# Kernel tuning notes

Hardware: AMD Instinct MI355X
Metric: run time of the kernel (lower is better)

## Reference

```python
import jax, jax.numpy as jnp
import numpy as np

B, C, N = 4, 256, 512
CQ = C // 4
SIGMA = 15.0
PICK = 0  # args.picked_point_num
FACTOR = 180.0 / (np.pi * SIGMA)
BN_EPS = 1e-5


def _angle_embed(angles, W, b):
    """SinusoidalPositionalEmbedding (interleaved sin/cos, detached) + Linear proj."""
    d = W.shape[0]
    div_term = jnp.exp(jnp.arange(0, d, 2, dtype=jnp.float32) * (-np.log(10000.0) / d))
    omegas = (angles * FACTOR)[..., None] * div_term  # (..., d/2)
    # torch cat([sin, cos], dim=2) on (-1, d/2, 1) then view -> interleaved [s0,c0,s1,c1,...]
    emb = jnp.stack([jnp.sin(omegas), jnp.cos(omegas)], axis=-1).reshape(*angles.shape, d)
    emb = jax.lax.stop_gradient(emb)  # .detach() in torch
    return emb @ W.T + b


def setup_inputs() -> dict:
    key = jax.random.key(0)
    ks = jax.random.split(key, 16)
    s = 0.05
    return {
        "x": jax.random.normal(ks[0], (B, C, N), jnp.float32),
        "pca": jax.random.normal(ks[1], (B, C, N), jnp.float32),
        "angle_lrf": jax.random.uniform(ks[2], (B, N, N), jnp.float32, 0.0, np.pi),
        "angle_pca": jax.random.uniform(ks[3], (B, N), jnp.float32, 0.0, np.pi),
        "Wkp": jax.random.normal(ks[4], (CQ, C), jnp.float32) * s,
        "Wk": jax.random.normal(ks[5], (CQ, C), jnp.float32) * s,
        "Wv": jax.random.normal(ks[6], (C, C), jnp.float32) * s,
        "Wvp": jax.random.normal(ks[7], (C, C), jnp.float32) * s,
        "emb1_W": jax.random.normal(ks[8], (CQ, CQ), jnp.float32) * s,
        "emb1_b": jnp.zeros((CQ,), jnp.float32),
        "emb2_W": jax.random.normal(ks[9], (CQ, CQ), jnp.float32) * s,
        "emb2_b": jnp.zeros((CQ,), jnp.float32),
        "lin_W": jax.random.normal(ks[10], (C, C), jnp.float32) * s,
        "lin_b": jnp.zeros((C,), jnp.float32),
        "bn_gamma": jnp.ones((C,), jnp.float32),
        "bn_beta": jnp.zeros((C,), jnp.float32),
    }


def reference(x, pca, angle_lrf, angle_pca, Wkp, Wk, Wv, Wvp,
              emb1_W, emb1_b, emb2_W, emb2_b, lin_W, lin_b, bn_gamma, bn_beta):
    # q uses the k_conv_pca weight (weight tying in __init__)
    x_q = jnp.einsum('oc,bcn->bno', Wkp, x)            # (B,N,CQ)
    k_lrf = jnp.einsum('oc,bcn->bon', Wk, x)           # (B,CQ,N)
    k_pca = jnp.einsum('oc,bcn->bon', Wkp, pca)        # (B,CQ,N)
    energy_lrf = jnp.einsum('bno,bom->bnm', x_q, k_lrf)
    energy_pca = jnp.einsum('bno,bom->bnm', x_q, k_pca)
    e1 = _angle_embed(angle_lrf, emb1_W, emb1_b)       # (B,N,N,CQ) relative-angle bias
    energy_lrf = energy_lrf + jnp.einsum('bnc,bnmc->bnm', x_q, e1)
    e2 = _angle_embed(angle_pca, emb2_W, emb2_b)       # (B,N,CQ)
    energy_pca = energy_pca + jnp.einsum('bnc,bmc->bnm', x_q, e2)
    energy = jax.nn.softmax(energy_lrf + energy_pca, axis=-1)
    # extra column renormalization
    energy = energy / (1e-12 + energy.sum(axis=1, keepdims=True))
    point_relation = energy[:, PICK:PICK + 1, :]       # (B,1,N)
    v_lrf = jnp.einsum('oc,bcn->bon', Wv, x)
    v_pca = jnp.einsum('oc,bcn->bon', Wvp, pca)
    x_lrf = jnp.einsum('bon,bnm->bom', v_lrf, energy)
    x_pca = jnp.einsum('bon,bnm->bom', v_pca, energy)
    x_r = 0.5 * x_lrf + 0.5 * x_pca
    z = jnp.einsum('oc,bcn->bon', lin_W, x - x_r) + lin_b[None, :, None]
    # BatchNorm1d (training-mode batch stats, biased var)
    mu = z.mean(axis=(0, 2), keepdims=True)
    var = z.var(axis=(0, 2), keepdims=True)
    y = bn_gamma[None, :, None] * (z - mu) * jax.lax.rsqrt(var + BN_EPS) + bn_beta[None, :, None]
    out = x + jax.nn.gelu(y, approximate=False)
    return out, point_relation
```

## Files before the change

### kernel.cpp

```cpp
#include <hip/hip_runtime.h>
#include <math.h>

#define FCT_REV 0.6079271018540267f
#define DIVK 0.28782313662425575f

using bf16x8 = __attribute__((ext_vector_type(8))) short;
using f32x4  = __attribute__((ext_vector_type(4))) float;

__device__ inline short f2bf(float f) {
    union { float f; unsigned u; } v; v.f = f;
    unsigned r = v.u + 0x7FFFu + ((v.u >> 16) & 1u);
    return (short)(r >> 16);
}
__device__ inline float bf2f(short s) {
    union { unsigned u; float f; } v;
    v.u = ((unsigned)(unsigned short)s) << 16;
    return v.f;
}
__device__ inline unsigned pk2(float lo, float hi) {
    return ((unsigned)(unsigned short)f2bf(hi) << 16) | (unsigned)(unsigned short)f2bf(lo);
}
__device__ inline float sinrev(float x) {
    float r; asm("v_sin_f32 %0, %1" : "=v"(r) : "v"(x)); return r;
}
__device__ inline float cosrev(float x) {
    float r; asm("v_cos_f32 %0, %1" : "=v"(r) : "v"(x)); return r;
}

__global__ __launch_bounds__(256) void k_prep(
    const float* __restrict__ Wkp, const float* __restrict__ Wk,
    const float* __restrict__ Wv, const float* __restrict__ Wvp,
    const float* __restrict__ linW, const float* __restrict__ e1W,
    const float* __restrict__ e2W,
    const float* __restrict__ x, const float* __restrict__ pca,
    short* __restrict__ Wcatb, short* __restrict__ InTb,
    float* __restrict__ e2Wt, float* __restrict__ stat, float* __restrict__ colsum)
{
    __shared__ float ts[64][65];
    const int bid = blockIdx.x;
    const int t = threadIdx.x;
    if (bid < 176) {
        if (bid == 0) {
            for (int i = t; i < 2048; i += 256) colsum[i] = 0.f;
            for (int i = t; i < 512; i += 256) stat[i] = 0.f;
        } else if (bid == 1) {
            for (int i = t; i < 4096; i += 256) {
                int k = i >> 6, o = i & 63;
                e2Wt[k*64 + o] = e2W[o*64 + k];
            }
        }
        #pragma unroll
        for (int rr = 0; rr < 4; ++rr) {
            const int r = bid*4 + rr;
            for (int k = t; k < 512; k += 256) {
                float v = 0.f;
                if (r < 64) { if (k < 256) v = Wkp[r*256 + k]; }
                else if (r < 128) { int o = r-64;  v = (k<256) ? Wk[o*256+k]  : Wkp[o*256 + k-256]; }
                else if (r < 384) { int o = r-128; v = (k<256) ? Wv[o*256+k]  : Wvp[o*256 + k-256]; }
                else if (r < 640) { int o = r-384; if (k<256) v = linW[o*256+k]; }
                else {
                    int o = r-640;
                    if (k < 256) {
                        float a = 0.f;
                        for (int j = 0; j < 64; ++j) a = fmaf(e1W[j*64 + o], Wkp[j*256 + k], a);
                        v = a;
                    }
                }
                Wcatb[(size_t)r*512 + k] = f2bf(v);
            }
        }
    } else {
        const int id = bid - 176;
        const int b  = id >> 6;
        const int kt = (id >> 3) & 7;
        const int nt = id & 7;
        const int k0 = kt*64, n0 = nt*64;
        const float* src = (k0 < 256) ? (x + ((size_t)b*256 + k0)*512)
                                      : (pca + ((size_t)b*256 + (k0-256))*512);
        #pragma unroll
        for (int i = 0; i < 16; ++i) {
            int idx = t + 256*i;
            int r = idx >> 6, c = idx & 63;
            ts[r][c] = src[(size_t)r*512 + n0 + c];
        }
        __syncthreads();
        short* dst = InTb + (size_t)b*512*512;
        #pragma unroll
        for (int i = 0; i < 16; ++i) {
            int idx = t + 256*i;
            int n = idx >> 6, k = idx & 63;
            dst[(size_t)(n0+n)*512 + k0 + k] = f2bf(ts[k][n]);
        }
    }
}

__global__ __launch_bounds__(256) void k_gemm1(
    const short* __restrict__ Wcatb, const short* __restrict__ InTb,
    const float* __restrict__ angle_pca, const float* __restrict__ e2Wt,
    short* __restrict__ xqb, short* __restrict__ KtT, short* __restrict__ vsumb,
    float* __restrict__ linx, float* __restrict__ q1T)
{
    __shared__ float embs[32][65];
    __shared__ float e2ws[64][64];
    const int bid = blockIdx.x;
    const int b  = bid / 176;
    const int rt = (bid / 16) % 11;
    const int ct = bid % 16;
    const int r0 = rt*64, c0 = ct*32;
    const int w = threadIdx.x >> 6, lane = threadIdx.x & 63;
    const int lr = lane & 15, lg = lane >> 4;
    const int t = threadIdx.x;

    if (r0 == 64) {
        const int mloc = t >> 3, q = t & 7;
        const float arev = angle_pca[b*512 + c0 + mloc] * FCT_REV;
        #pragma unroll
        for (int j = q*4; j < q*4+4; ++j) {
            const float arg = arev * __expf(-(float)j * DIVK);
            embs[mloc][2*j]   = sinrev(arg);
            embs[mloc][2*j+1] = cosrev(arg);
        }
        #pragma unroll
        for (int i = 0; i < 16; ++i) {
            const int idx = t + 256*i;
            e2ws[idx >> 6][idx & 63] = e2Wt[idx];
        }
    }

    const short* ap  = Wcatb + (size_t)(r0 + w*16 + lr)*512 + 8*lg;
    const short* bp0 = InTb + (size_t)b*512*512 + (size_t)(c0 + lr)*512 + 8*lg;
    const short* bp1 = bp0 + 16*512;

    f32x4 acc0 = {0.f,0.f,0.f,0.f}, acc1 = {0.f,0.f,0.f,0.f};
    #pragma unroll 4
    for (int kk = 0; kk < 512; kk += 32) {
        bf16x8 a  = *(const bf16x8*)(ap  + kk);
        bf16x8 b0 = *(const bf16x8*)(bp0 + kk);
        bf16x8 b1 = *(const bf16x8*)(bp1 + kk);
        acc0 = __builtin_amdgcn_mfma_f32_16x16x32_bf16(a, b0, acc0, 0, 0, 0);
        acc1 = __builtin_amdgcn_mfma_f32_16x16x32_bf16(a, b1, acc1, 0, 0, 0);
    }
    const int rowb = r0 + w*16 + lg*4;
    const int col0 = c0 + lr;
    if (r0 == 0) {
        #pragma unroll
        for (int j = 0; j < 4; ++j) {
            xqb[((size_t)b*512 + col0)*64 + rowb + j]      = f2bf(acc0[j]);
            xqb[((size_t)b*512 + col0 + 16)*64 + rowb + j] = f2bf(acc1[j]);
        }
    } else if (r0 == 64) {
        __syncthreads();
        const int o0 = w*16 + lg*4;
        float e[8];
        #pragma unroll
        for (int i = 0; i < 8; ++i) e[i] = 0.f;
        #pragma unroll 8
        for (int k = 0; k < 64; ++k) {
            const float em0 = embs[lr][k];
            const float em1 = embs[lr + 16][k];
            #pragma unroll
            for (int j = 0; j < 4; ++j) {
                const float wv = e2ws[k][o0 + j];
                e[j]     = fmaf(wv, em0, e[j]);
                e[4 + j] = fmaf(wv, em1, e[4 + j]);
            }
        }
        uint2 u0, u1;
        u0.x = pk2(acc0[0] + e[0], acc0[1] + e[1]);
        u0.y = pk2(acc0[2] + e[2], acc0[3] + e[3]);
        u1.x = pk2(acc1[0] + e[4], acc1[1] + e[5]);
        u1.y = pk2(acc1[2] + e[6], acc1[3] + e[7]);
        *(uint2*)(KtT + ((size_t)b*512 + col0)*64 + o0)      = u0;
        *(uint2*)(KtT + ((size_t)b*512 + col0 + 16)*64 + o0) = u1;
    } else if (r0 < 384) {
        #pragma unroll
        for (int j = 0; j < 4; ++j) {
            vsumb[((size_t)b*256 + rowb-128 + j)*512 + col0]      = f2bf(acc0[j]);
            vsumb[((size_t)b*256 + rowb-128 + j)*512 + col0 + 16] = f2bf(acc1[j]);
        }
    } else if (r0 < 640) {
        #pragma unroll
        for (int j = 0; j < 4; ++j) {
            linx[((size_t)b*256 + rowb-384 + j)*512 + col0]      = acc0[j];
            linx[((size_t)b*256 + rowb-384 + j)*512 + col0 + 16] = acc1[j];
        }
    } else {
        #pragma unroll
        for (int j = 0; j < 4; ++j) {
            q1T[((size_t)b*512 + col0)*64 + rowb-640 + j]      = acc0[j];
            q1T[((size_t)b*512 + col0 + 16)*64 + rowb-640 + j] = acc1[j];
        }
    }
}

__global__ __launch_bounds__(256) void k_qk(
    const short* __restrict__ xqb, const short* __restrict__ KtT,
    float* __restrict__ S)
{
    const int bid = blockIdx.x;
    const int b  = bid / 128;
    const int rt = (bid / 16) % 8;
    const int ct = bid % 16;
    const int r0 = rt*64, c0 = ct*32;
    const int w = threadIdx.x >> 6, lane = threadIdx.x & 63;
    const int lr = lane & 15, lg = lane >> 4;
    const short* ap  = xqb + ((size_t)b*512 + r0 + w*16 + lr)*64 + 8*lg;
    const short* bp0 = KtT + ((size_t)b*512 + c0 + lr)*64 + 8*lg;
    const short* bp1 = bp0 + 16*64;
    f32x4 acc0 = {0.f,0.f,0.f,0.f}, acc1 = {0.f,0.f,0.f,0.f};
    #pragma unroll
    for (int kk = 0; kk < 64; kk += 32) {
        bf16x8 a  = *(const bf16x8*)(ap  + kk);
        bf16x8 b0 = *(const bf16x8*)(bp0 + kk);
        bf16x8 b1 = *(const bf16x8*)(bp1 + kk);
        acc0 = __builtin_amdgcn_mfma_f32_16x16x32_bf16(a, b0, acc0, 0, 0, 0);
        acc1 = __builtin_amdgcn_mfma_f32_16x16x32_bf16(a, b1, acc1, 0, 0, 0);
    }
    const int rowb = r0 + w*16 + lg*4;
    const int col0 = c0 + lr;
    float* Sb = S + (size_t)b*512*512;
    #pragma unroll
    for (int j = 0; j < 4; ++j) {
        Sb[(size_t)(rowb+j)*512 + col0]      = acc0[j];
        Sb[(size_t)(rowb+j)*512 + col0 + 16] = acc1[j];
    }
}

__global__ __launch_bounds__(256) void k_energy2(
    const float* __restrict__ S, const float* __restrict__ q1T,
    const float* __restrict__ angle_lrf, short* __restrict__ ETb,
    float* __restrict__ colsum)
{
    const int b  = blockIdx.x >> 7;
    const int n0 = (blockIdx.x & 127) * 4;
    __shared__ float qs[4][64];
    __shared__ float divs[32];
    __shared__ float4 xw[4];
    const int t = threadIdx.x;
    if (t < 64) {
        #pragma unroll
        for (int i = 0; i < 4; ++i) qs[i][t] = q1T[((size_t)b*512 + n0 + i)*64 + t];
    } else if (t < 96) {
        divs[t-64] = __expf(-(float)(t-64) * DIVK);
    }
    __syncthreads();
    float acc[4][2], av[4][2];
    #pragma unroll
    for (int i = 0; i < 4; ++i) {
        const float2 sv = *(const float2*)&S[((size_t)b*512 + n0 + i)*512 + 2*t];
        const float2 an = *(const float2*)&angle_lrf[((size_t)b*512 + n0 + i)*512 + 2*t];
        acc[i][0] = sv.x; acc[i][1] = sv.y;
        av[i][0] = an.x * FCT_REV; av[i][1] = an.y * FCT_REV;
    }
    #pragma unroll 2
    for (int j = 0; j < 32; ++j) {
        const float d = divs[j];
        #pragma unroll
        for (int i = 0; i < 4; ++i) {
            const float q0 = qs[i][2*j], q1 = qs[i][2*j+1];
            #pragma unroll
            for (int m = 0; m < 2; ++m) {
                const float arg = av[i][m] * d;
                acc[i][m] = fmaf(q0, sinrev(arg), fmaf(q1, cosrev(arg), acc[i][m]));
            }
        }
    }
    float v0 = fmaxf(acc[0][0], acc[0][1]), v1 = fmaxf(acc[1][0], acc[1][1]);
    float v2 = fmaxf(acc[2][0], acc[2][1]), v3 = fmaxf(acc[3][0], acc[3][1]);
    #pragma unroll
    for (int off = 1; off < 64; off <<= 1) {
        v0 = fmaxf(v0, __shfl_xor(v0, off));
        v1 = fmaxf(v1, __shfl_xor(v1, off));
        v2 = fmaxf(v2, __shfl_xor(v2, off));
        v3 = fmaxf(v3, __shfl_xor(v3, off));
    }
    const int wid = t >> 6, lane = t & 63;
    if (lane == 0) { float4 f = {v0,v1,v2,v3}; xw[wid] = f; }
    __syncthreads();
    {
        const float4 a0 = xw[0], a1 = xw[1], a2 = xw[2], a3 = xw[3];
        v0 = fmaxf(fmaxf(a0.x,a1.x), fmaxf(a2.x,a3.x));
        v1 = fmaxf(fmaxf(a0.y,a1.y), fmaxf(a2.y,a3.y));
        v2 = fmaxf(fmaxf(a0.z,a1.z), fmaxf(a2.z,a3.z));
        v3 = fmaxf(fmaxf(a0.w,a1.w), fmaxf(a2.w,a3.w));
    }
    float p[4][2];
    p[0][0] = __expf(acc[0][0]-v0); p[0][1] = __expf(acc[0][1]-v0);
    p[1][0] = __expf(acc[1][0]-v1); p[1][1] = __expf(acc[1][1]-v1);
    p[2][0] = __expf(acc[2][0]-v2); p[2][1] = __expf(acc[2][1]-v2);
    p[3][0] = __expf(acc[3][0]-v3); p[3][1] = __expf(acc[3][1]-v3);
    float s0 = p[0][0]+p[0][1], s1 = p[1][0]+p[1][1];
    float s2 = p[2][0]+p[2][1], s3 = p[3][0]+p[3][1];
    #pragma unroll
    for (int off = 1; off < 64; off <<= 1) {
        s0 += __shfl_xor(s0, off); s1 += __shfl_xor(s1, off);
        s2 += __shfl_xor(s2, off); s3 += __shfl_xor(s3, off);
    }
    __syncthreads();
    if (lane == 0) { float4 f = {s0,s1,s2,s3}; xw[wid] = f; }
    __syncthreads();
    {
        const float4 a0 = xw[0], a1 = xw[1], a2 = xw[2], a3 = xw[3];
        s0 = (a0.x+a1.x) + (a2.x+a3.x);
        s1 = (a0.y+a1.y) + (a2.y+a3.y);
        s2 = (a0.z+a1.z) + (a2.z+a3.z);
        s3 = (a0.w+a1.w) + (a2.w+a3.w);
    }
    const float i0 = 1.f/s0, i1 = 1.f/s1, i2 = 1.f/s2, i3 = 1.f/s3;
    short* Eb = ETb + (size_t)b*512*512;
    #pragma unroll
    for (int m = 0; m < 2; ++m) {
        const float e0 = p[0][m]*i0, e1 = p[1][m]*i1, e2 = p[2][m]*i2, e3 = p[3][m]*i3;
        uint2 u;
        u.x = pk2(e0, e1);
        u.y = pk2(e2, e3);
        *(uint2*)(Eb + (size_t)(2*t + m)*512 + n0) = u;
        atomicAdd(&colsum[b*512 + 2*t + m], (e0 + e1) + (e2 + e3));
    }
}

__global__ __launch_bounds__(256) void k_xr2(
    const short* __restrict__ vsumb, const short* __restrict__ ETb,
    const float* __restrict__ colsum, short* __restrict__ xrT,
    float* __restrict__ out)
{
    const int bid = blockIdx.x;
    const int b  = bid / 64;
    const int rt = (bid / 16) % 4;
    const int ct = bid % 16;
    const int r0 = rt*64, c0 = ct*32;
    const int w = threadIdx.x >> 6, lane = threadIdx.x & 63;
    const int lr = lane & 15, lg = lane >> 4;
    const short* ap  = vsumb + (size_t)b*256*512 + (size_t)(r0 + w*16 + lr)*512 + 8*lg;
    const short* bp0 = ETb + (size_t)b*512*512 + (size_t)(c0 + lr)*512 + 8*lg;
    const short* bp1 = bp0 + 16*512;
    f32x4 acc0 = {0.f,0.f,0.f,0.f}, acc1 = {0.f,0.f,0.f,0.f};
    #pragma unroll 4
    for (int kk = 0; kk < 512; kk += 32) {
        bf16x8 a  = *(const bf16x8*)(ap  + kk);
        bf16x8 b0 = *(const bf16x8*)(bp0 + kk);
        bf16x8 b1 = *(const bf16x8*)(bp1 + kk);
        acc0 = __builtin_amdgcn_mfma_f32_16x16x32_bf16(a, b0, acc0, 0, 0, 0);
        acc1 = __builtin_amdgcn_mfma_f32_16x16x32_bf16(a, b1, acc1, 0, 0, 0);
    }
    const int rowb = r0 + w*16 + lg*4;
    const int m0 = c0 + lr, m1 = m0 + 16;
    const float rc0 = 1.f / (1e-12f + colsum[b*512 + m0]);
    const float rc1 = 1.f / (1e-12f + colsum[b*512 + m1]);
    const float s0 = 0.5f * rc0, s1 = 0.5f * rc1;
    short* xb = xrT + (size_t)b*512*256;
    uint2 u;
    u.x = pk2(acc0[0]*s0, acc0[1]*s0);
    u.y = pk2(acc0[2]*s0, acc0[3]*s0);
    *(uint2*)(xb + (size_t)m0*256 + rowb) = u;
    u.x = pk2(acc1[0]*s1, acc1[1]*s1);
    u.y = pk2(acc1[2]*s1, acc1[3]*s1);
    *(uint2*)(xb + (size_t)m1*256 + rowb) = u;
    if (w == 0 && lg == 0) {
        out[(size_t)4*256*512 + b*512 + m0] = bf2f(ETb[((size_t)b*512 + m0)*512]) * rc0;
        out[(size_t)4*256*512 + b*512 + m1] = bf2f(ETb[((size_t)b*512 + m1)*512]) * rc1;
    }
}

__global__ __launch_bounds__(256) void k_z2st(
    const short* __restrict__ Wcatb, const short* __restrict__ xrT,
    const float* __restrict__ linx, const float* __restrict__ lin_b,
    float* __restrict__ z, float* __restrict__ stat)
{
    const int bid = blockIdx.x;
    const int b  = bid / 64;
    const int rt = (bid / 16) % 4;
    const int ct = bid % 16;
    const int r0 = rt*64, c0 = ct*32;
    const int w = threadIdx.x >> 6, lane = threadIdx.x & 63;
    const int lr = lane & 15, lg = lane >> 4;
    const short* ap  = Wcatb + (size_t)(384 + r0 + w*16 + lr)*512 + 8*lg;
    const short* bp0 = xrT + (size_t)b*512*256 + (size_t)(c0 + lr)*256 + 8*lg;
    const short* bp1 = bp0 + 16*256;
    f32x4 acc0 = {0.f,0.f,0.f,0.f}, acc1 = {0.f,0.f,0.f,0.f};
    #pragma unroll
    for (int kk = 0; kk < 256; kk += 32) {
        bf16x8 a  = *(const bf16x8*)(ap  + kk);
        bf16x8 b0 = *(const bf16x8*)(bp0 + kk);
        bf16x8 b1 = *(const bf16x8*)(bp1 + kk);
        acc0 = __builtin_amdgcn_mfma_f32_16x16x32_bf16(a, b0, acc0, 0, 0, 0);
        acc1 = __builtin_amdgcn_mfma_f32_16x16x32_bf16(a, b1, acc1, 0, 0, 0);
    }
    const int rowb = r0 + w*16 + lg*4;
    const int col0 = c0 + lr;
    const float* Lb = linx + (size_t)b*256*512;
    float* zb = z + (size_t)b*256*512;
    #pragma unroll
    for (int j = 0; j < 4; ++j) {
        const float lb = lin_b[rowb+j];
        const float z0 = Lb[(size_t)(rowb+j)*512 + col0]      - acc0[j] + lb;
        const float z1 = Lb[(size_t)(rowb+j)*512 + col0 + 16] - acc1[j] + lb;
        zb[(size_t)(rowb+j)*512 + col0]      = z0;
        zb[(size_t)(rowb+j)*512 + col0 + 16] = z1;
        float s  = z0 + z1;
        float s2 = z0*z0 + z1*z1;
        #pragma unroll
        for (int off = 1; off < 16; off <<= 1) {
            s  += __shfl_xor(s,  off);
            s2 += __shfl_xor(s2, off);
        }
        if (lr == 0) {
            atomicAdd(&stat[rowb+j], s);
            atomicAdd(&stat[256 + rowb+j], s2);
        }
    }
}

__global__ __launch_bounds__(256) void k_final(
    const float* __restrict__ x, const float* __restrict__ z,
    const float* __restrict__ stat, const float* __restrict__ gamma,
    const float* __restrict__ beta, float* __restrict__ out)
{
    const int gid = blockIdx.x*256 + threadIdx.x;
    const int base = gid * 4;
    const int c = (base >> 9) & 255;
    const float mu  = stat[c] * (1.f/2048.f);
    const float var = stat[256 + c] * (1.f/2048.f) - mu*mu;
    const float gsc = gamma[c] * rsqrtf(var + 1e-5f);
    const float bt  = beta[c];
    const float4 zv = *(const float4*)&z[base];
    const float4 xv = *(const float4*)&x[base];
    float4 ov;
    {
        float y = (zv.x - mu)*gsc + bt;
        ov.x = xv.x + 0.5f*y*(1.f + erff(y*0.70710678118654752f));
        y = (zv.y - mu)*gsc + bt;
        ov.y = xv.y + 0.5f*y*(1.f + erff(y*0.70710678118654752f));
        y = (zv.z - mu)*gsc + bt;
        ov.z = xv.z + 0.5f*y*(1.f + erff(y*0.70710678118654752f));
        y = (zv.w - mu)*gsc + bt;
        ov.w = xv.w + 0.5f*y*(1.f + erff(y*0.70710678118654752f));
    }
    *(float4*)&out[base] = ov;
}

extern "C" void kernel_launch(void* const* d_in, const int* in_sizes, int n_in,
                              void* d_out, int out_size, void* d_ws, size_t ws_size,
                              hipStream_t stream)
{
    const float* x         = (const float*)d_in[0];
    const float* pca       = (const float*)d_in[1];
    const float* angle_lrf = (const float*)d_in[2];
    const float* angle_pca = (const float*)d_in[3];
    const float* Wkp       = (const float*)d_in[4];
    const float* Wk        = (const float*)d_in[5];
    const float* Wv        = (const float*)d_in[6];
    const float* Wvp       = (const float*)d_in[7];
    const float* e1W       = (const float*)d_in[8];
    const float* e2W       = (const float*)d_in[10];
    const float* linW      = (const float*)d_in[12];
    const float* linb      = (const float*)d_in[13];
    const float* gamma     = (const float*)d_in[14];
    const float* beta      = (const float*)d_in[15];

    char* w = (char*)d_ws;
    short* Wcatb  = (short*)(w + 0);
    short* InTb   = (short*)(w + 720896);
    short* vsumb  = (short*)(w + 2818048);
    short* KtT    = (short*)(w + 3866624);
    short* ETb    = (short*)(w + 4128768);
    short* xrT    = (short*)(w + 6225920);
    float* stat   = (float*)(w + 7274496);
    float* colsum = (float*)(w + 7276544);
    float* S      = (float*)(w + 7284736);
    float* e2Wt   = (float*)(w + 7284736);
    float* z      = (float*)(w + 7284736);
    short* xqb    = (short*)(w + 12003328);
    float* q1T    = (float*)(w + 12265472);
    float* linx   = (float*)(w + 12789760);
    float* out    = (float*)d_out;

    k_prep   <<<432, 256, 0, stream>>>(Wkp, Wk, Wv, Wvp, linW, e1W, e2W, x, pca,
                                       Wcatb, InTb, e2Wt, stat, colsum);
    k_gemm1  <<<704, 256, 0, stream>>>(Wcatb, InTb, angle_pca, e2Wt,
                                       xqb, KtT, vsumb, linx, q1T);
    k_qk     <<<512, 256, 0, stream>>>(xqb, KtT, S);
    k_energy2<<<512, 256, 0, stream>>>(S, q1T, angle_lrf, ETb, colsum);
    k_xr2    <<<256, 256, 0, stream>>>(vsumb, ETb, colsum, xrT, out);
    k_z2st   <<<256, 256, 0, stream>>>(Wcatb, xrT, linx, linb, z, stat);
    k_final  <<<512, 256, 0, stream>>>(x, z, stat, gamma, beta, out);
}
```

Baseline: 81.53 us.

## Fuse QK score computation into energy kernel, removing S intermediate

```diff
diff --git a/kernel.cpp b/kernel.cpp
--- a/kernel.cpp
+++ b/kernel.cpp
@@ -193,129 +193,113 @@
     }
 }
 
-__global__ __launch_bounds__(256) void k_qk(
+__global__ __launch_bounds__(256) void k_energy2(
     const short* __restrict__ xqb, const short* __restrict__ KtT,
-    float* __restrict__ S)
-{
-    const int bid = blockIdx.x;
-    const int b  = bid / 128;
-    const int rt = (bid / 16) % 8;
-    const int ct = bid % 16;
-    const int r0 = rt*64, c0 = ct*32;
-    const int w = threadIdx.x >> 6, lane = threadIdx.x & 63;
-    const int lr = lane & 15, lg = lane >> 4;
-    const short* ap  = xqb + ((size_t)b*512 + r0 + w*16 + lr)*64 + 8*lg;
-    const short* bp0 = KtT + ((size_t)b*512 + c0 + lr)*64 + 8*lg;
-    const short* bp1 = bp0 + 16*64;
-    f32x4 acc0 = {0.f,0.f,0.f,0.f}, acc1 = {0.f,0.f,0.f,0.f};
-    #pragma unroll
-    for (int kk = 0; kk < 64; kk += 32) {
-        bf16x8 a  = *(const bf16x8*)(ap  + kk);
-        bf16x8 b0 = *(const bf16x8*)(bp0 + kk);
-        bf16x8 b1 = *(const bf16x8*)(bp1 + kk);
-        acc0 = __builtin_amdgcn_mfma_f32_16x16x32_bf16(a, b0, acc0, 0, 0, 0);
-        acc1 = __builtin_amdgcn_mfma_f32_16x16x32_bf16(a, b1, acc1, 0, 0, 0);
-    }
-    const int rowb = r0 + w*16 + lg*4;
-    const int col0 = c0 + lr;
-    float* Sb = S + (size_t)b*512*512;
-    #pragma unroll
-    for (int j = 0; j < 4; ++j) {
-        Sb[(size_t)(rowb+j)*512 + col0]      = acc0[j];
-        Sb[(size_t)(rowb+j)*512 + col0 + 16] = acc1[j];
-    }
-}
-
-__global__ __launch_bounds__(256) void k_energy2(
-    const float* __restrict__ S, const float* __restrict__ q1T,
-    const float* __restrict__ angle_lrf, short* __restrict__ ETb,
-    float* __restrict__ colsum)
-{
-    const int b  = blockIdx.x >> 7;
-    const int n0 = (blockIdx.x & 127) * 4;
-    __shared__ float qs[4][64];
+    const float* __restrict__ q1T, const float* __restrict__ angle_lrf,
+    short* __restrict__ ETb, float* __restrict__ colsum)
+{
+    const int b  = blockIdx.x >> 8;
+    const int n0 = (blockIdx.x & 255) * 2;
+    __shared__ float xqf[2][64];
+    __shared__ float qs[2][64];
     __shared__ float divs[32];
-    __shared__ float4 xw[4];
+    __shared__ float2 xw[4];
     const int t = threadIdx.x;
     if (t < 64) {
-        #pragma unroll
-        for (int i = 0; i < 4; ++i) qs[i][t] = q1T[((size_t)b*512 + n0 + i)*64 + t];
+        xqf[0][t] = bf2f(xqb[((size_t)b*512 + n0)*64 + t]);
+        xqf[1][t] = bf2f(xqb[((size_t)b*512 + n0 + 1)*64 + t]);
+        qs[0][t]  = q1T[((size_t)b*512 + n0)*64 + t];
+        qs[1][t]  = q1T[((size_t)b*512 + n0 + 1)*64 + t];
     } else if (t < 96) {
         divs[t-64] = __expf(-(float)(t-64) * DIVK);
     }
     __syncthreads();
-    float acc[4][2], av[4][2];
-    #pragma unroll
-    for (int i = 0; i < 4; ++i) {
-        const float2 sv = *(const float2*)&S[((size_t)b*512 + n0 + i)*512 + 2*t];
-        const float2 an = *(const float2*)&angle_lrf[((size_t)b*512 + n0 + i)*512 + 2*t];
-        acc[i][0] = sv.x; acc[i][1] = sv.y;
-        av[i][0] = an.x * FCT_REV; av[i][1] = an.y * FCT_REV;
-    }
+    float acc[2][2];
+    #pragma unroll
+    for (int mi = 0; mi < 2; ++mi) {
+        const int m = t + mi*256;
+        const short* kp = KtT + ((size_t)b*512 + m)*64;
+        float a0 = 0.f, a1 = 0.f;
+        #pragma unroll
+        for (int o8 = 0; o8 < 64; o8 += 8) {
+            const uint4 u = *(const uint4*)(kp + o8);
+            const float4 xa0 = *(const float4*)&xqf[0][o8];
+            const float4 xb0 = *(const float4*)&xqf[0][o8+4];
+            const float4 xa1 = *(const float4*)&xqf[1][o8];
+            const float4 xb1 = *(const float4*)&xqf[1][o8+4];
+            union { unsigned q; float f; } e0,e1,e2,e3,e4,e5,e6,e7;
+            e0.q = u.x << 16; e1.q = u.x & 0xFFFF0000u;
+            e2.q = u.y << 16; e3.q = u.y & 0xFFFF0000u;
+            e4.q = u.z << 16; e5.q = u.z & 0xFFFF0000u;
+            e6.q = u.w << 16; e7.q = u.w & 0xFFFF0000u;
+            a0 = fmaf(e0.f, xa0.x, a0); a0 = fmaf(e1.f, xa0.y, a0);
+            a0 = fmaf(e2.f, xa0.z, a0); a0 = fmaf(e3.f, xa0.w, a0);
+            a0 = fmaf(e4.f, xb0.x, a0); a0 = fmaf(e5.f, xb0.y, a0);
+            a0 = fmaf(e6.f, xb0.z, a0); a0 = fmaf(e7.f, xb0.w, a0);
+            a1 = fmaf(e0.f, xa1.x, a1); a1 = fmaf(e1.f, xa1.y, a1);
+            a1 = fmaf(e2.f, xa1.z, a1); a1 = fmaf(e3.f, xa1.w, a1);
+            a1 = fmaf(e4.f, xb1.x, a1); a1 = fmaf(e5.f, xb1.y, a1);
+            a1 = fmaf(e6.f, xb1.z, a1); a1 = fmaf(e7.f, xb1.w, a1);
+        }
+        acc[0][mi] = a0; acc[1][mi] = a1;
+    }
+    float av[2][2];
+    av[0][0] = angle_lrf[((size_t)b*512 + n0)*512 + t] * FCT_REV;
+    av[0][1] = angle_lrf[((size_t)b*512 + n0)*512 + t + 256] * FCT_REV;
+    av[1][0] = angle_lrf[((size_t)b*512 + n0 + 1)*512 + t] * FCT_REV;
+    av[1][1] = angle_lrf[((size_t)b*512 + n0 + 1)*512 + t + 256] * FCT_REV;
     #pragma unroll 2
     for (int j = 0; j < 32; ++j) {
         const float d = divs[j];
         #pragma unroll
-        for (int i = 0; i < 4; ++i) {
-            const float q0 = qs[i][2*j], q1 = qs[i][2*j+1];
+        for (int r = 0; r < 2; ++r) {
+            const float q0 = qs[r][2*j], q1v = qs[r][2*j+1];
             #pragma unroll
-            for (int m = 0; m < 2; ++m) {
-                const float arg = av[i][m] * d;
-                acc[i][m] = fmaf(q0, sinrev(arg), fmaf(q1, cosrev(arg), acc[i][m]));
+            for (int mi = 0; mi < 2; ++mi) {
+                const float arg = av[r][mi] * d;
+                acc[r][mi] = fmaf(q0, sinrev(arg), fmaf(q1v, cosrev(arg), acc[r][mi]));
             }
         }
     }
-    float v0 = fmaxf(acc[0][0], acc[0][1]), v1 = fmaxf(acc[1][0], acc[1][1]);
-    float v2 = fmaxf(acc[2][0], acc[2][1]), v3 = fmaxf(acc[3][0], acc[3][1]);
+    float v0 = fmaxf(acc[0][0], acc[0][1]);
+    float v1 = fmaxf(acc[1][0], acc[1][1]);
     #pragma unroll
     for (int off = 1; off < 64; off <<= 1) {
         v0 = fmaxf(v0, __shfl_xor(v0, off));
         v1 = fmaxf(v1, __shfl_xor(v1, off));
-        v2 = fmaxf(v2, __shfl_xor(v2, off));
-        v3 = fmaxf(v3, __shfl_xor(v3, off));
     }
     const int wid = t >> 6, lane = t & 63;
-    if (lane == 0) { float4 f = {v0,v1,v2,v3}; xw[wid] = f; }
+    if (lane == 0) { float2 f = {v0, v1}; xw[wid] = f; }
     __syncthreads();
     {
-        const float4 a0 = xw[0], a1 = xw[1], a2 = xw[2], a3 = xw[3];
+        const float2 a0 = xw[0], a1 = xw[1], a2 = xw[2], a3 = xw[3];
         v0 = fmaxf(fmaxf(a0.x,a1.x), fmaxf(a2.x,a3.x));
         v1 = fmaxf(fmaxf(a0.y,a1.y), fmaxf(a2.y,a3.y));
-        v2 = fmaxf(fmaxf(a0.z,a1.z), fmaxf(a2.z,a3.z));
-        v3 = fmaxf(fmaxf(a0.w,a1.w), fmaxf(a2.w,a3.w));
-    }
-    float p[4][2];
+    }
+    float p[2][2];
     p[0][0] = __expf(acc[0][0]-v0); p[0][1] = __expf(acc[0][1]-v0);
     p[1][0] = __expf(acc[1][0]-v1); p[1][1] = __expf(acc[1][1]-v1);
-    p[2][0] = __expf(acc[2][0]-v2); p[2][1] = __expf(acc[2][1]-v2);
-    p[3][0] = __expf(acc[3][0]-v3); p[3][1] = __expf(acc[3][1]-v3);
     float s0 = p[0][0]+p[0][1], s1 = p[1][0]+p[1][1];
-    float s2 = p[2][0]+p[2][1], s3 = p[3][0]+p[3][1];
     #pragma unroll
     for (int off = 1; off < 64; off <<= 1) {
         s0 += __shfl_xor(s0, off); s1 += __shfl_xor(s1, off);
-        s2 += __shfl_xor(s2, off); s3 += __shfl_xor(s3, off);
     }
     __syncthreads();
-    if (lane == 0) { float4 f = {s0,s1,s2,s3}; xw[wid] = f; }
+    if (lane == 0) { float2 f = {s0, s1}; xw[wid] = f; }
     __syncthreads();
     {
-        const float4 a0 = xw[0], a1 = xw[1], a2 = xw[2], a3 = xw[3];
+        const float2 a0 = xw[0], a1 = xw[1], a2 = xw[2], a3 = xw[3];
         s0 = (a0.x+a1.x) + (a2.x+a3.x);
         s1 = (a0.y+a1.y) + (a2.y+a3.y);
-        s2 = (a0.z+a1.z) + (a2.z+a3.z);
-        s3 = (a0.w+a1.w) + (a2.w+a3.w);
-    }
-    const float i0 = 1.f/s0, i1 = 1.f/s1, i2 = 1.f/s2, i3 = 1.f/s3;
+    }
+    const float i0 = 1.f/s0, i1 = 1.f/s1;
     short* Eb = ETb + (size_t)b*512*512;
     #pragma unroll
-    for (int m = 0; m < 2; ++m) {
-        const float e0 = p[0][m]*i0, e1 = p[1][m]*i1, e2 = p[2][m]*i2, e3 = p[3][m]*i3;
-        uint2 u;
-        u.x = pk2(e0, e1);
-        u.y = pk2(e2, e3);
-        *(uint2*)(Eb + (size_t)(2*t + m)*512 + n0) = u;
-        atomicAdd(&colsum[b*512 + 2*t + m], (e0 + e1) + (e2 + e3));
+    for (int mi = 0; mi < 2; ++mi) {
+        const int m = t + mi*256;
+        const float e0 = p[0][mi]*i0, e1 = p[1][mi]*i1;
+        *(unsigned*)(Eb + (size_t)m*512 + n0) = pk2(e0, e1);
+        atomicAdd(&colsum[b*512 + m], e0 + e1);
     }
 }
 
@@ -467,7 +451,6 @@
     short* xrT    = (short*)(w + 6225920);
     float* stat   = (float*)(w + 7274496);
     float* colsum = (float*)(w + 7276544);
-    float* S      = (float*)(w + 7284736);
     float* e2Wt   = (float*)(w + 7284736);
     float* z      = (float*)(w + 7284736);
     short* xqb    = (short*)(w + 12003328);
@@ -475,13 +458,12 @@
     float* linx   = (float*)(w + 12789760);
     float* out    = (float*)d_out;
 
-    k_prep   <<<432, 256, 0, stream>>>(Wkp, Wk, Wv, Wvp, linW, e1W, e2W, x, pca,
-                                       Wcatb, InTb, e2Wt, stat, colsum);
-    k_gemm1  <<<704, 256, 0, stream>>>(Wcatb, InTb, angle_pca, e2Wt,
-                                       xqb, KtT, vsumb, linx, q1T);
-    k_qk     <<<512, 256, 0, stream>>>(xqb, KtT, S);
-    k_energy2<<<512, 256, 0, stream>>>(S, q1T, angle_lrf, ETb, colsum);
-    k_xr2    <<<256, 256, 0, stream>>>(vsumb, ETb, colsum, xrT, out);
-    k_z2st   <<<256, 256, 0, stream>>>(Wcatb, xrT, linx, linb, z, stat);
-    k_final  <<<512, 256, 0, stream>>>(x, z, stat, gamma, beta, out);
-}
+    k_prep   <<<432,  256, 0, stream>>>(Wkp, Wk, Wv, Wvp, linW, e1W, e2W, x, pca,
+                                        Wcatb, InTb, e2Wt, stat, colsum);
+    k_gemm1  <<<704,  256, 0, stream>>>(Wcatb, InTb, angle_pca, e2Wt,
+                                        xqb, KtT, vsumb, linx, q1T);
+    k_energy2<<<1024, 256, 0, stream>>>(xqb, KtT, q1T, angle_lrf, ETb, colsum);
+    k_xr2    <<<256,  256, 0, stream>>>(vsumb, ETb, colsum, xrT, out);
+    k_z2st   <<<256,  256, 0, stream>>>(Wcatb, xrT, linx, linb, z, stat);
+    k_final  <<<512,  256, 0, stream>>>(x, z, stat, gamma, beta, out);
+}
```

New measurement: 87.18 us. 6.9% more time.
